# Kernel optimization log

Measured on AMD Instinct MI355X. Metric: run time of the kernel, lower is better.

Reference implementation:

```python
import jax, jax.numpy as jnp
import numpy as np

GRID_SIZE = 5
SPLINE_ORDER = 3
GRID_MIN, GRID_MAX = -1.0, 1.0
LN_EPS = 1e-5


def _make_grid():
    # Extended knot grid shared across input features: (grid_size + 2*order + 1,)
    h = (GRID_MAX - GRID_MIN) / GRID_SIZE
    return jnp.arange(-SPLINE_ORDER, GRID_SIZE + SPLINE_ORDER + 1, dtype=jnp.float32) * h + GRID_MIN


def b_splines(x, grid):
    # x: (B, in) -> bases: (B, in, grid_size + spline_order)
    xe = x[..., None]  # (B, in, 1)
    bases = ((xe >= grid[:-1]) & (xe < grid[1:])).astype(x.dtype)
    for k in range(1, SPLINE_ORDER + 1):
        left = (xe - grid[: -(k + 1)]) / (grid[k:-1] - grid[: -(k + 1)])
        right = (grid[k + 1:] - xe) / (grid[k + 1:] - grid[1:-k])
        bases = left * bases[..., :-1] + right * bases[..., 1:]
    return bases


def setup_inputs() -> dict:
    key = jax.random.key(0)
    ks = jax.random.split(key, 5)
    B, IN, OUT, COEF = 16384, 1024, 512, GRID_SIZE + SPLINE_ORDER
    return {
        "rgb_features": jax.random.normal(ks[0], (B, IN // 2), jnp.float32),
        "tactile_features": jax.random.normal(ks[1], (B, IN // 2), jnp.float32),
        "base_weight": jax.random.normal(ks[2], (OUT, IN), jnp.float32) * 0.02,
        "spline_weight": jax.random.normal(ks[3], (OUT, IN, COEF), jnp.float32) * 0.02,
        "spline_scaler": 1.0 + 0.02 * jax.random.normal(ks[4], (OUT, IN), jnp.float32),
        "ln_gamma": jnp.ones((OUT,), jnp.float32),
        "ln_beta": jnp.zeros((OUT,), jnp.float32),
    }


def reference(rgb_features, tactile_features, base_weight, spline_weight, spline_scaler, ln_gamma, ln_beta):
    x = jnp.concatenate((rgb_features, tactile_features), axis=1)  # (B, 1024)
    grid = _make_grid()
    # KANLinear: base path (SiLU + linear) + spline path (B-spline basis + linear)
    base_out = jnp.einsum("bi,oi->bo", jax.nn.silu(x), base_weight)
    bases = b_splines(x, grid)  # (B, in, coef)
    scaled_w = spline_weight * spline_scaler[..., None]  # (out, in, coef)
    spline_out = jnp.einsum("bik,oik->bo", bases, scaled_w)
    fused = base_out + spline_out
    # LayerNorm over last dim
    mu = jnp.mean(fused, axis=-1, keepdims=True)
    var = jnp.var(fused, axis=-1, keepdims=True)
    fused = (fused - mu) * jax.lax.rsqrt(var + LN_EPS) * ln_gamma + ln_beta
    # Dropout is identity in eval mode
    return fused
```

## Files before the change

### kernel.cpp

```cpp
#include <hip/hip_runtime.h>
#include <cstdint>
#include <cstddef>


#define BATCH    16384
#define OUT_DIM  512
#define KTOT     9216
#define BM       128
#define BK       64
#define NCHUNK        144
#define SPLINE_CHUNKS 128

typedef __attribute__((ext_vector_type(8))) short  short8;
typedef __attribute__((ext_vector_type(4))) float  f32x4;

static __device__ __forceinline__ unsigned short f2bf(float f) {
    unsigned int u = __float_as_uint(f);
    unsigned int r = u + 0x7fffu + ((u >> 16) & 1u);
    return (unsigned short)(r >> 16);
}

__global__ void prep_w_kernel(const float* __restrict__ bw,
                              const float* __restrict__ sw,
                              const float* __restrict__ sc,
                              unsigned short* __restrict__ Wp) {
    int t = blockIdx.x * 256 + threadIdx.x;
    int o = t / 1152;
    int g = t - o * 1152;
    int sz = o & 7;
    unsigned short o8[8];
    size_t dst;
    if (g < 1024) {
        float s = sc[(size_t)o * 1024 + g];
        const float* w = sw + ((size_t)o * 1024 + g) * 8;
        #pragma unroll
        for (int k = 0; k < 8; ++k) o8[k] = f2bf(w[k] * s);
        dst = (size_t)o * KTOT + (size_t)(g >> 3) * 64 + (size_t)(((g & 7) ^ sz)) * 8;
    } else {
        int gi = g - 1024;
        const float* w = bw + (size_t)o * 1024 + gi * 8;
        #pragma unroll
        for (int k = 0; k < 8; ++k) o8[k] = f2bf(w[k]);
        dst = (size_t)o * KTOT + (size_t)8192 + (size_t)(gi >> 3) * 64 + (size_t)(((gi & 7) ^ sz)) * 8;
    }
    *reinterpret_cast<short8*>(Wp + dst) = *reinterpret_cast<const short8*>(o8);
}

static __device__ __forceinline__ void basis8(float x, unsigned* out) {
    float tpos = (x + 2.2f) * 2.5f;
    float fj   = floorf(tpos);
    int   j    = (int)fj;
    float u  = tpos - fj;
    float v  = 1.f - u;
    float u2 = u * u;
    float u3 = u2 * u;
    const float c6 = 1.f / 6.f;
    float n0 = v * v * v * c6;
    float n3 = u3 * c6;
    float n1 = __builtin_fmaf(0.5f, u3, __builtin_fmaf(-1.f, u2, 4.f * c6));
    float n2 = 1.f - n0 - n1 - n3;
    unsigned p0, p1;
    asm("v_cvt_pk_bf16_f32 %0, %1, %2" : "=v"(p0) : "v"(n0), "v"(n1));
    asm("v_cvt_pk_bf16_f32 %0, %1, %2" : "=v"(p1) : "v"(n2), "v"(n3));
    int sh = (j << 4) - 48;
    int c  = sh & 16;
    int w  = (sh - c) >> 5;
    unsigned long long P = ((unsigned long long)p1 << 32) | p0;
    unsigned long long T = P << c;
    unsigned t0 = (unsigned)T;
    unsigned t1 = (unsigned)(T >> 32);
    unsigned t2 = c ? (p1 >> 16) : 0u;
    #pragma unroll
    for (int i = 0; i < 4; ++i) {
        unsigned r = 0u;
        r = (w == i    ) ? t0 : r;
        r = (w == i - 1) ? t1 : r;
        r = (w == i - 2) ? t2 : r;
        out[i] = r;
    }
}

template<bool SPLIT>
__launch_bounds__(512, 2)
__global__ void kan_gemm_kernel(const float* __restrict__ rgb,
                                const float* __restrict__ tac,
                                const unsigned short* __restrict__ Wp,
                                float* __restrict__ dest_base) {
    __shared__ unsigned short At[2][BM][BK];
    __shared__ unsigned short Bt[2][OUT_DIM][BK];

    const int tid  = threadIdx.x;
    const int lane = tid & 63;
    const int wid  = tid >> 6;
    const int b0   = blockIdx.x * BM;
    const int ksp  = SPLIT ? (int)blockIdx.y : 0;
    const int kc0  = SPLIT ? (ksp ? 72 : 0)             : 0;
    const int kcS  = SPLIT ? (ksp ? SPLINE_CHUNKS : 72) : SPLINE_CHUNKS;
    const int kc1  = SPLIT ? (ksp ? NCHUNK : 72)        : NCHUNK;
    float* dest = dest_base + (size_t)ksp * BATCH * OUT_DIM;

    f32x4 acc[8][4];
    #pragma unroll
    for (int m = 0; m < 8; ++m)
        #pragma unroll
        for (int n = 0; n < 4; ++n)
            acc[m][n] = (f32x4){0.f, 0.f, 0.f, 0.f};

    auto mfma_step = [&](int ab, int bb) {
        #pragma unroll
        for (int ks = 0; ks < 2; ++ks) {
            int cb = ks * 4 + (lane >> 4);
            short8 afr[8];
            #pragma unroll
            for (int m = 0; m < 8; ++m) {
                int row = m * 16 + (lane & 15);
                afr[m] = *reinterpret_cast<const short8*>(&At[ab][row][(cb ^ (row & 7)) * 8]);
            }
            #pragma unroll
            for (int n = 0; n < 4; ++n) {
                int row = wid * 64 + n * 16 + (lane & 15);
                short8 bfr = *reinterpret_cast<const short8*>(
                    &Bt[bb][row][(cb ^ (row & 7)) * 8]);
                #pragma unroll
                for (int m = 0; m < 8; ++m)
                    acc[m][n] = __builtin_amdgcn_mfma_f32_16x16x32_bf16(
                        afr[m], bfr, acc[m][n], 0, 0, 0);
            }
        }
    };

    auto loadx_s = [&](int c, float* xv) {
        int i0 = c * 8;
        const float* xs = (i0 < 512) ? rgb : tac;
        int ic = i0 & 511;
        #pragma unroll
        for (int rep = 0; rep < 2; ++rep) {
            int e = tid + rep * 512;
            xv[rep] = xs[(size_t)(b0 + (e >> 3)) * 512 + ic + (e & 7)];
        }
    };

    auto loadx_b = [&](int c, f32x4* xq) {
        int i0 = (c - SPLINE_CHUNKS) * 64;
        const float* xs = (i0 < 512) ? rgb : tac;
        int ic = i0 & 511;
        #pragma unroll
        for (int rep = 0; rep < 2; ++rep) {
            int gq = tid + rep * 512;
            const float* xp = xs + (size_t)(b0 + (gq >> 3)) * 512 + ic + (gq & 7) * 8;
            xq[rep * 2]     = *reinterpret_cast<const f32x4*>(xp);
            xq[rep * 2 + 1] = *reinterpret_cast<const f32x4*>(xp + 4);
        }
    };

    auto silupack = [&](const f32x4& xa, const f32x4& xb, unsigned* o) {
        float s[8];
        #pragma unroll
        for (int q = 0; q < 4; ++q) {
            float a = xa[q];
            s[q]     = a * __builtin_amdgcn_rcpf(1.f + __expf(-a));
            float b = xb[q];
            s[q + 4] = b * __builtin_amdgcn_rcpf(1.f + __expf(-b));
        }
        #pragma unroll
        for (int q = 0; q < 4; ++q)
            asm("v_cvt_pk_bf16_f32 %0, %1, %2"
                : "=v"(o[q]) : "v"(s[2 * q]), "v"(s[2 * q + 1]));
    };

    auto writeA = [&](const unsigned* o8, int ab) {
        #pragma unroll
        for (int rep = 0; rep < 2; ++rep) {
            int e = tid + rep * 512;
            int r = e >> 3;
            int c = e & 7;
            *reinterpret_cast<short8*>(&At[ab][r][(c ^ (r & 7)) * 8]) =
                *reinterpret_cast<const short8*>(o8 + rep * 4);
        }
    };

    auto gload_B = [&](int kc, int buf) {
        int k0g = kc * BK;
        #pragma unroll
        for (int rp = 0; rp < 8; ++rp) {
            int row0 = wid * 64 + rp * 8;
            const unsigned short* gp =
                Wp + (size_t)(row0 + (lane >> 3)) * KTOT + k0g + (lane & 7) * 8;
            __builtin_amdgcn_global_load_lds(
                (const __attribute__((address_space(1))) unsigned int*)gp,
                (__attribute__((address_space(3))) unsigned int*)&Bt[buf][row0][0],
                16, 0, 0);
        }
    };

    float xv0[2];
    loadx_s(kc0, xv0);
    gload_B(kc0, 0);
    gload_B(kc0 + 1 < kc1 ? kc0 + 1 : kc1 - 1, 1);
    float xn[2] = {0.f, 0.f};
    if (kc0 + 1 < kcS) loadx_s(kc0 + 1, xn);
    {
        unsigned o8[8];
        basis8(xv0[0], o8);
        basis8(xv0[1], o8 + 4);
        writeA(o8, 0);
    }
    asm volatile("s_waitcnt vmcnt(10) lgkmcnt(0)" ::: "memory");
    __builtin_amdgcn_sched_barrier(0);
    __builtin_amdgcn_s_barrier();
    __builtin_amdgcn_sched_barrier(0);

    for (int t = kc0; t < kcS; ++t) {
        const int  buf   = (t - kc0) & 1;
        const bool moreA = (t + 1 < kcS);
        unsigned o8[8];
        if (moreA) {
            basis8(xn[0], o8);
            basis8(xn[1], o8 + 4);
            writeA(o8, buf ^ 1);
        }
        if (t + 2 < kcS) loadx_s(t + 2, xn);
        mfma_step(buf, buf);
        __builtin_amdgcn_sched_barrier(0);
        __builtin_amdgcn_s_barrier();
        __builtin_amdgcn_sched_barrier(0);
        int tn = (t + 2 < kc1) ? t + 2 : kc1 - 1;
        gload_B(tn, buf);
        asm volatile("s_waitcnt vmcnt(10) lgkmcnt(0)" ::: "memory");
        __builtin_amdgcn_sched_barrier(0);
        __builtin_amdgcn_s_barrier();
        __builtin_amdgcn_sched_barrier(0);
    }

    if (kcS < kc1) {
        f32x4 xq[4];
        {
            f32x4 x0[4];
            loadx_b(kcS, x0);
            unsigned o8[8];
            silupack(x0[0], x0[1], o8);
            silupack(x0[2], x0[3], o8 + 4);
            writeA(o8, (kcS - kc0) & 1);
            if (kcS + 1 < kc1) loadx_b(kcS + 1, xq);
            asm volatile("s_waitcnt lgkmcnt(0)" ::: "memory");
            __builtin_amdgcn_sched_barrier(0);
            __builtin_amdgcn_s_barrier();
            __builtin_amdgcn_sched_barrier(0);
        }
        for (int t = kcS; t < kc1; ++t) {
            const int  buf   = (t - kc0) & 1;
            const bool moreA = (t + 1 < kc1);
            const bool moreX = (t + 2 < kc1);
            unsigned o8[8];
            if (moreA) {
                silupack(xq[0], xq[1], o8);
                silupack(xq[2], xq[3], o8 + 4);
                writeA(o8, buf ^ 1);
            }
            f32x4 nq[4];
            if (moreX) loadx_b(t + 2, nq);
            mfma_step(buf, buf);
            __builtin_amdgcn_sched_barrier(0);
            __builtin_amdgcn_s_barrier();
            __builtin_amdgcn_sched_barrier(0);
            int tn = moreX ? t + 2 : kc1 - 1;
            gload_B(tn, buf);
            asm volatile("s_waitcnt vmcnt(12) lgkmcnt(0)" ::: "memory");
            __builtin_amdgcn_sched_barrier(0);
            __builtin_amdgcn_s_barrier();
            __builtin_amdgcn_sched_barrier(0);
            if (moreX) {
                #pragma unroll
                for (int q = 0; q < 4; ++q) xq[q] = nq[q];
            }
        }
    }

    #pragma unroll
    for (int m = 0; m < 8; ++m) {
        int row = b0 + m * 16 + ((lane >> 4) << 2);
        #pragma unroll
        for (int n = 0; n < 4; ++n) {
            int col = wid * 64 + n * 16 + (lane & 15);
            #pragma unroll
            for (int jj = 0; jj < 4; ++jj)
                dest[(size_t)(row + jj) * OUT_DIM + col] = acc[m][n][jj];
        }
    }
}

__global__ void reduce_ln_kernel(const float* __restrict__ P0,
                                 const float* __restrict__ P1,
                                 const float* __restrict__ gamma,
                                 const float* __restrict__ beta,
                                 float* __restrict__ out) {
    int row  = blockIdx.x * 4 + (threadIdx.x >> 6);
    int lane = threadIdx.x & 63;
    const float* p0 = P0 + (size_t)row * OUT_DIM;
    const float* p1 = P1 + (size_t)row * OUT_DIM;
    f32x4 a0 = *reinterpret_cast<const f32x4*>(p0 + lane * 4);
    f32x4 a1 = *reinterpret_cast<const f32x4*>(p0 + 256 + lane * 4);
    f32x4 b0 = *reinterpret_cast<const f32x4*>(p1 + lane * 4);
    f32x4 b1 = *reinterpret_cast<const f32x4*>(p1 + 256 + lane * 4);
    f32x4 v0, v1;
    #pragma unroll
    for (int q = 0; q < 4; ++q) { v0[q] = a0[q] + b0[q]; v1[q] = a1[q] + b1[q]; }
    float s = 0.f, ss = 0.f;
    #pragma unroll
    for (int q = 0; q < 4; ++q) {
        s  += v0[q] + v1[q];
        ss += v0[q] * v0[q] + v1[q] * v1[q];
    }
    #pragma unroll
    for (int off = 1; off < 64; off <<= 1) {
        s  += __shfl_xor(s, off);
        ss += __shfl_xor(ss, off);
    }
    float mu  = s * (1.f / 512.f);
    float var = ss * (1.f / 512.f) - mu * mu;
    float rs  = rsqrtf(var + 1e-5f);
    f32x4 g0 = *reinterpret_cast<const f32x4*>(gamma + lane * 4);
    f32x4 g1 = *reinterpret_cast<const f32x4*>(gamma + 256 + lane * 4);
    f32x4 e0 = *reinterpret_cast<const f32x4*>(beta + lane * 4);
    f32x4 e1 = *reinterpret_cast<const f32x4*>(beta + 256 + lane * 4);
    float* po = out + (size_t)row * OUT_DIM;
    f32x4 r0, r1;
    #pragma unroll
    for (int q = 0; q < 4; ++q) {
        r0[q] = (v0[q] - mu) * rs * g0[q] + e0[q];
        r1[q] = (v1[q] - mu) * rs * g1[q] + e1[q];
    }
    *reinterpret_cast<f32x4*>(po + lane * 4)       = r0;
    *reinterpret_cast<f32x4*>(po + 256 + lane * 4) = r1;
}

__global__ void ln_kernel(float* __restrict__ io,
                          const float* __restrict__ gamma,
                          const float* __restrict__ beta) {
    int row  = blockIdx.x * 4 + (threadIdx.x >> 6);
    int lane = threadIdx.x & 63;
    float* p = io + (size_t)row * OUT_DIM;
    f32x4 v0 = *reinterpret_cast<const f32x4*>(p + lane * 4);
    f32x4 v1 = *reinterpret_cast<const f32x4*>(p + 256 + lane * 4);
    float s = 0.f, ss = 0.f;
    #pragma unroll
    for (int q = 0; q < 4; ++q) {
        s  += v0[q] + v1[q];
        ss += v0[q] * v0[q] + v1[q] * v1[q];
    }
    #pragma unroll
    for (int off = 1; off < 64; off <<= 1) {
        s  += __shfl_xor(s, off);
        ss += __shfl_xor(ss, off);
    }
    float mu  = s * (1.f / 512.f);
    float var = ss * (1.f / 512.f) - mu * mu;
    float rs  = rsqrtf(var + 1e-5f);
    f32x4 g0 = *reinterpret_cast<const f32x4*>(gamma + lane * 4);
    f32x4 g1 = *reinterpret_cast<const f32x4*>(gamma + 256 + lane * 4);
    f32x4 e0 = *reinterpret_cast<const f32x4*>(beta + lane * 4);
    f32x4 e1 = *reinterpret_cast<const f32x4*>(beta + 256 + lane * 4);
    f32x4 r0, r1;
    #pragma unroll
    for (int q = 0; q < 4; ++q) {
        r0[q] = (v0[q] - mu) * rs * g0[q] + e0[q];
        r1[q] = (v1[q] - mu) * rs * g1[q] + e1[q];
    }
    *reinterpret_cast<f32x4*>(p + lane * 4)       = r0;
    *reinterpret_cast<f32x4*>(p + 256 + lane * 4) = r1;
}

extern "C" void kernel_launch(void* const* d_in, const int* in_sizes, int n_in,
                              void* d_out, int out_size, void* d_ws, size_t ws_size,
                              hipStream_t stream) {
    const float* rgb   = (const float*)d_in[0];
    const float* tac   = (const float*)d_in[1];
    const float* bw    = (const float*)d_in[2];
    const float* sw    = (const float*)d_in[3];
    const float* sc    = (const float*)d_in[4];
    const float* gamma = (const float*)d_in[5];
    const float* beta  = (const float*)d_in[6];
    float* out = (float*)d_out;
    unsigned short* Wp = (unsigned short*)d_ws;

    prep_w_kernel<<<2304, 256, 0, stream>>>(bw, sw, sc, Wp);

    const size_t PART = (size_t)BATCH * OUT_DIM * sizeof(float);
    const size_t POFF = 16ull << 20;
    if (ws_size >= POFF + 2 * PART) {
        float* P = (float*)((char*)d_ws + POFF);
        dim3 g(BATCH / BM, 2);
        kan_gemm_kernel<true><<<g, 512, 0, stream>>>(rgb, tac, Wp, P);
        reduce_ln_kernel<<<BATCH / 4, 256, 0, stream>>>(
            P, P + (size_t)BATCH * OUT_DIM, gamma, beta, out);
    } else {
        dim3 g(BATCH / BM, 1);
        kan_gemm_kernel<false><<<g, 512, 0, stream>>>(rgb, tac, Wp, out);
        ln_kernel<<<BATCH / 4, 256, 0, stream>>>(out, gamma, beta);
    }
}
```

Measured before the change: 195.8 us.

## Retile warps to 2x4 grid and interleave LDS reads with MFMA phases

Changes the per-warp tile from 128x64 to 64x128 (2 row groups by 4 column groups), which lowers LDS fragment reads per MFMA. Each K step is split into four phases separated by barriers, and s_setprio raises priority around the MFMA bursts. Basis or SiLU computation and the A-tile writes are spread across those phases so they overlap with the matrix math. B prefetch depth drops from two chunks ahead to one with a full vmcnt(0) wait, and the many extra barriers may add stall time.

Result: slower. 208.0 us (+6.2%).

```diff
diff --git a/kernel.cpp b/kernel.cpp
--- a/kernel.cpp
+++ b/kernel.cpp
@@ -80,6 +80,12 @@
     }
 }
 
+#define PHASE_PRE()  do { __builtin_amdgcn_s_barrier(); \
+    asm volatile("s_waitcnt lgkmcnt(0)" ::: "memory"); \
+    __builtin_amdgcn_sched_barrier(0); } while (0)
+#define PHASE_POST() do { __builtin_amdgcn_sched_barrier(0); \
+    __builtin_amdgcn_s_barrier(); } while (0)
+
 template<bool SPLIT>
 __launch_bounds__(512, 2)
 __global__ void kan_gemm_kernel(const float* __restrict__ rgb,
@@ -93,40 +99,46 @@
     const int lane = tid & 63;
     const int wid  = tid >> 6;
     const int b0   = blockIdx.x * BM;
+    const int wr   = wid & 1;
+    const int wc   = wid >> 1;
     const int ksp  = SPLIT ? (int)blockIdx.y : 0;
     const int kc0  = SPLIT ? (ksp ? 72 : 0)             : 0;
     const int kcS  = SPLIT ? (ksp ? SPLINE_CHUNKS : 72) : SPLINE_CHUNKS;
     const int kc1  = SPLIT ? (ksp ? NCHUNK : 72)        : NCHUNK;
     float* dest = dest_base + (size_t)ksp * BATCH * OUT_DIM;
 
-    f32x4 acc[8][4];
-    #pragma unroll
-    for (int m = 0; m < 8; ++m)
+    f32x4 acc[4][8];
+    #pragma unroll
+    for (int m = 0; m < 4; ++m)
+        #pragma unroll
+        for (int n = 0; n < 8; ++n)
+            acc[m][n] = (f32x4){0.f, 0.f, 0.f, 0.f};
+
+    auto readA = [&](short8* Af, int ab, int ks) {
+        int cb = ks * 4 + (lane >> 4);
+        #pragma unroll
+        for (int m = 0; m < 4; ++m) {
+            int row = wr * 64 + m * 16 + (lane & 15);
+            Af[m] = *reinterpret_cast<const short8*>(&At[ab][row][(cb ^ (row & 7)) * 8]);
+        }
+    };
+    auto readB = [&](short8* Bf, int bb, int ks, int nh) {
+        int cb = ks * 4 + (lane >> 4);
+        #pragma unroll
+        for (int n = 0; n < 4; ++n) {
+            int row = wc * 128 + (nh + n) * 16 + (lane & 15);
+            Bf[n] = *reinterpret_cast<const short8*>(&Bt[bb][row][(cb ^ (row & 7)) * 8]);
+        }
+    };
+    auto mfma16 = [&](const short8* Af, const short8* Bf, int nh) {
+        __builtin_amdgcn_s_setprio(1);
         #pragma unroll
         for (int n = 0; n < 4; ++n)
-            acc[m][n] = (f32x4){0.f, 0.f, 0.f, 0.f};
-
-    auto mfma_step = [&](int ab, int bb) {
-        #pragma unroll
-        for (int ks = 0; ks < 2; ++ks) {
-            int cb = ks * 4 + (lane >> 4);
-            short8 afr[8];
             #pragma unroll
-            for (int m = 0; m < 8; ++m) {
-                int row = m * 16 + (lane & 15);
-                afr[m] = *reinterpret_cast<const short8*>(&At[ab][row][(cb ^ (row & 7)) * 8]);
-            }
-            #pragma unroll
-            for (int n = 0; n < 4; ++n) {
-                int row = wid * 64 + n * 16 + (lane & 15);
-                short8 bfr = *reinterpret_cast<const short8*>(
-                    &Bt[bb][row][(cb ^ (row & 7)) * 8]);
-                #pragma unroll
-                for (int m = 0; m < 8; ++m)
-                    acc[m][n] = __builtin_amdgcn_mfma_f32_16x16x32_bf16(
-                        afr[m], bfr, acc[m][n], 0, 0, 0);
-            }
-        }
+            for (int m = 0; m < 4; ++m)
+                acc[m][nh + n] = __builtin_amdgcn_mfma_f32_16x16x32_bf16(
+                    Af[m], Bf[n], acc[m][nh + n], 0, 0, 0);
+        __builtin_amdgcn_s_setprio(0);
     };
 
     auto loadx_s = [&](int c, float* xv) {
@@ -139,7 +151,6 @@
             xv[rep] = xs[(size_t)(b0 + (e >> 3)) * 512 + ic + (e & 7)];
         }
     };
-
     auto loadx_b = [&](int c, f32x4* xq) {
         int i0 = (c - SPLINE_CHUNKS) * 64;
         const float* xs = (i0 < 512) ? rgb : tac;
@@ -152,7 +163,6 @@
             xq[rep * 2 + 1] = *reinterpret_cast<const f32x4*>(xp + 4);
         }
     };
-
     auto silupack = [&](const f32x4& xa, const f32x4& xb, unsigned* o) {
         float s[8];
         #pragma unroll
@@ -167,7 +177,6 @@
             asm("v_cvt_pk_bf16_f32 %0, %1, %2"
                 : "=v"(o[q]) : "v"(s[2 * q]), "v"(s[2 * q + 1]));
     };
-
     auto writeA = [&](const unsigned* o8, int ab) {
         #pragma unroll
         for (int rep = 0; rep < 2; ++rep) {
@@ -178,7 +187,6 @@
                 *reinterpret_cast<const short8*>(o8 + rep * 4);
         }
     };
-
     auto gload_B = [&](int kc, int buf) {
         int k0g = kc * BK;
         #pragma unroll
@@ -193,43 +201,54 @@
         }
     };
 
-    float xv0[2];
-    loadx_s(kc0, xv0);
-    gload_B(kc0, 0);
-    gload_B(kc0 + 1 < kc1 ? kc0 + 1 : kc1 - 1, 1);
-    float xn[2] = {0.f, 0.f};
-    if (kc0 + 1 < kcS) loadx_s(kc0 + 1, xn);
+    float xc[2];
     {
+        float x0[2];
+        loadx_s(kc0, x0);
+        gload_B(kc0, 0);
         unsigned o8[8];
-        basis8(xv0[0], o8);
-        basis8(xv0[1], o8 + 4);
+        basis8(x0[0], o8);
+        basis8(x0[1], o8 + 4);
         writeA(o8, 0);
-    }
-    asm volatile("s_waitcnt vmcnt(10) lgkmcnt(0)" ::: "memory");
-    __builtin_amdgcn_sched_barrier(0);
-    __builtin_amdgcn_s_barrier();
-    __builtin_amdgcn_sched_barrier(0);
-
-    for (int t = kc0; t < kcS; ++t) {
-        const int  buf   = (t - kc0) & 1;
-        const bool moreA = (t + 1 < kcS);
-        unsigned o8[8];
-        if (moreA) {
-            basis8(xn[0], o8);
-            basis8(xn[1], o8 + 4);
-            writeA(o8, buf ^ 1);
-        }
-        if (t + 2 < kcS) loadx_s(t + 2, xn);
-        mfma_step(buf, buf);
+        loadx_s(kc0 + 1 < kcS ? kc0 + 1 : kcS - 1, xc);
+        asm volatile("s_waitcnt vmcnt(0) lgkmcnt(0)" ::: "memory");
         __builtin_amdgcn_sched_barrier(0);
         __builtin_amdgcn_s_barrier();
         __builtin_amdgcn_sched_barrier(0);
-        int tn = (t + 2 < kc1) ? t + 2 : kc1 - 1;
-        gload_B(tn, buf);
-        asm volatile("s_waitcnt vmcnt(10) lgkmcnt(0)" ::: "memory");
-        __builtin_amdgcn_sched_barrier(0);
-        __builtin_amdgcn_s_barrier();
-        __builtin_amdgcn_sched_barrier(0);
+    }
+
+    for (int t = kc0; t < kcS; ++t) {
+        const int  buf   = (t - kc0) & 1;
+        const int  nbuf  = buf ^ 1;
+        const bool moreA = (t + 1 < kcS);
+        short8 Af[4], Bf[4];
+        unsigned o8[8];
+        float xn2[2];
+        readA(Af, buf, 0);
+        readB(Bf, buf, 0, 0);
+        loadx_s(t + 2 < kcS ? t + 2 : kcS - 1, xn2);
+        gload_B(t + 1 < kc1 ? t + 1 : kc1 - 1, nbuf);
+        PHASE_PRE();
+        mfma16(Af, Bf, 0);
+        PHASE_POST();
+        readB(Bf, buf, 0, 4);
+        if (moreA) basis8(xc[0], o8);
+        PHASE_PRE();
+        mfma16(Af, Bf, 4);
+        PHASE_POST();
+        readA(Af, buf, 1);
+        readB(Bf, buf, 1, 0);
+        if (moreA) basis8(xc[1], o8 + 4);
+        PHASE_PRE();
+        mfma16(Af, Bf, 0);
+        PHASE_POST();
+        readB(Bf, buf, 1, 4);
+        if (moreA) writeA(o8, nbuf);
+        PHASE_PRE();
+        mfma16(Af, Bf, 4);
+        asm volatile("s_waitcnt vmcnt(0)" ::: "memory");
+        PHASE_POST();
+        xc[0] = xn2[0]; xc[1] = xn2[1];
     }
 
     if (kcS < kc1) {
@@ -241,7 +260,7 @@
             silupack(x0[0], x0[1], o8);
             silupack(x0[2], x0[3], o8 + 4);
             writeA(o8, (kcS - kc0) & 1);
-            if (kcS + 1 < kc1) loadx_b(kcS + 1, xq);
+            loadx_b(kcS + 1 < kc1 ? kcS + 1 : kc1 - 1, xq);
             asm volatile("s_waitcnt lgkmcnt(0)" ::: "memory");
             __builtin_amdgcn_sched_barrier(0);
             __builtin_amdgcn_s_barrier();
@@ -249,39 +268,46 @@
         }
         for (int t = kcS; t < kc1; ++t) {
             const int  buf   = (t - kc0) & 1;
+            const int  nbuf  = buf ^ 1;
             const bool moreA = (t + 1 < kc1);
-            const bool moreX = (t + 2 < kc1);
+            short8 Af[4], Bf[4];
             unsigned o8[8];
-            if (moreA) {
-                silupack(xq[0], xq[1], o8);
-                silupack(xq[2], xq[3], o8 + 4);
-                writeA(o8, buf ^ 1);
-            }
-            f32x4 nq[4];
-            if (moreX) loadx_b(t + 2, nq);
-            mfma_step(buf, buf);
-            __builtin_amdgcn_sched_barrier(0);
-            __builtin_amdgcn_s_barrier();
-            __builtin_amdgcn_sched_barrier(0);
-            int tn = moreX ? t + 2 : kc1 - 1;
-            gload_B(tn, buf);
-            asm volatile("s_waitcnt vmcnt(12) lgkmcnt(0)" ::: "memory");
-            __builtin_amdgcn_sched_barrier(0);
-            __builtin_amdgcn_s_barrier();
-            __builtin_amdgcn_sched_barrier(0);
-            if (moreX) {
-                #pragma unroll
-                for (int q = 0; q < 4; ++q) xq[q] = nq[q];
-            }
-        }
-    }
-
-    #pragma unroll
-    for (int m = 0; m < 8; ++m) {
-        int row = b0 + m * 16 + ((lane >> 4) << 2);
-        #pragma unroll
-        for (int n = 0; n < 4; ++n) {
-            int col = wid * 64 + n * 16 + (lane & 15);
+            f32x4 xn2[4];
+            readA(Af, buf, 0);
+            readB(Bf, buf, 0, 0);
+            loadx_b(t + 2 < kc1 ? t + 2 : kc1 - 1, xn2);
+            gload_B(t + 1 < kc1 ? t + 1 : kc1 - 1, nbuf);
+            PHASE_PRE();
+            mfma16(Af, Bf, 0);
+            PHASE_POST();
+            readB(Bf, buf, 0, 4);
+            if (moreA) silupack(xq[0], xq[1], o8);
+            PHASE_PRE();
+            mfma16(Af, Bf, 4);
+            PHASE_POST();
+            readA(Af, buf, 1);
+            readB(Bf, buf, 1, 0);
+            if (moreA) silupack(xq[2], xq[3], o8 + 4);
+            PHASE_PRE();
+            mfma16(Af, Bf, 0);
+            PHASE_POST();
+            readB(Bf, buf, 1, 4);
+            if (moreA) writeA(o8, nbuf);
+            PHASE_PRE();
+            mfma16(Af, Bf, 4);
+            asm volatile("s_waitcnt vmcnt(0)" ::: "memory");
+            PHASE_POST();
+            #pragma unroll
+            for (int q = 0; q < 4; ++q) xq[q] = xn2[q];
+        }
+    }
+
+    #pragma unroll
+    for (int m = 0; m < 4; ++m) {
+        int row = b0 + wr * 64 + m * 16 + ((lane >> 4) << 2);
+        #pragma unroll
+        for (int n = 0; n < 8; ++n) {
+            int col = wc * 128 + n * 16 + (lane & 15);
             #pragma unroll
             for (int jj = 0; jj < 4; ++jj)
                 dest[(size_t)(row + jj) * OUT_DIM + col] = acc[m][n][jj];
```
